# Performance work log

Hardware: AMD Instinct MI355X
Metric: run time of the kernel (lower is better)

Reference implementation:

```python
import jax, jax.numpy as jnp
import numpy as np

N_TAPS = 2
N_DELAY = 1
N_ITER = 3
EPS_MODEL = 1e-5   # LaplaceModel clamp eps (eps_models['laplace'])
EPS = 1e-3         # ISS divide/clamp eps


def mag_sq(x):
    return jnp.real(x) ** 2 + jnp.imag(x) ** 2


def laplace_weights(X):
    # Laplace source model: w[..., c, n] = 1 / (2 * ||X[..., c, :, n]||_2), broadcast over freq
    # X: (..., c, f, n) complex -> weights: (..., c, 1, n) real
    denom = 2.0 * jnp.sqrt(jnp.sum(mag_sq(X), axis=-2, keepdims=True))
    return 1.0 / jnp.maximum(denom, EPS_MODEL)


def iss_type1(src, Xc, weights):
    # Equation (9): update vector for source `src`
    Xs = Xc[..., src, :, :]  # (..., f, n)
    v_num = jnp.mean(weights * Xc * jnp.conj(Xs)[..., None, :, :], axis=-1)  # (..., c, f)
    v_denom = jnp.mean(weights * mag_sq(Xs)[..., None, :, :], axis=-1)       # (..., c, f) real
    v = v_num / jnp.maximum(v_denom, EPS)
    v_s = 1.0 - 1.0 / jnp.sqrt(jnp.maximum(v_denom[..., src, :], EPS))
    v = v.at[..., src, :].set(v_s.astype(v.dtype))
    return v


def iss_type2(src, tap, Xc, X_bar, weights):
    # update vector for dereverberation tap (src, tap)
    Xst = X_bar[..., src, :, tap, :]  # (..., f, n)
    v_num = jnp.mean(weights * Xc * jnp.conj(Xst)[..., None, :, :], axis=-1)
    # NOTE: the source code does NOT apply the 1/n_frames norm to v_denom here
    v_denom = jnp.sum(weights * mag_sq(Xst)[..., None, :, :], axis=-1)
    return v_num / jnp.maximum(v_denom, EPS)


def epoch_update(Xloc, Xc, W, X_bar, n_chan):
    weights = laplace_weights(Xloc)  # (..., c, 1, n)
    g = jnp.maximum(jnp.mean(mag_sq(Xloc), axis=(-2, -1), keepdims=True), 1e-5)
    Xloc = Xloc / jnp.sqrt(g)
    weights = weights * g
    for src in range(n_chan):
        v = iss_type1(src, Xc, weights)  # (..., c, f)
        Xc = Xc - v[..., None] * Xc[..., src, :, :][..., None, :, :]
        W = W - v[..., None] * W[..., src, :, :][..., None, :, :]
    for src in range(n_chan):
        for tap in range(N_TAPS):
            v = iss_type2(src, tap, Xc, X_bar, weights)
            Xc = Xc - v[..., None] * X_bar[..., src, :, tap, :][..., None, :, :]
    return Xloc, Xc, W


def auxiva_t_iss(X):
    batch = X.shape[:-3]
    n_chan, n_freq, n_frames = X.shape[-3:]
    T, D = N_TAPS, N_DELAY
    # hankel view of left-padded signal; keep only the T oldest rows (delayed taps)
    X_pad = jnp.pad(X, [(0, 0)] * (X.ndim - 1) + [(T + D, 0)])
    # X_bar: (..., c, f, T, n), X_bar[..., tap, t] = X[..., t - (T + D) + tap]
    X_bar = jnp.stack([X_pad[..., t:t + n_frames] for t in range(T)], axis=-2)
    eye = jnp.eye(n_chan, dtype=X.dtype)
    W = jnp.broadcast_to(eye[:, None, :], batch + (n_chan, n_freq, n_chan))
    Xloc = X  # the (buggy-but-faithful) local X that only gets renormalized each epoch
    Xc = X    # self.X, the demixed signal updated by ISS
    for _ in range(N_ITER):
        Xloc, Xc, W = epoch_update(Xloc, Xc, W, X_bar, n_chan)
    # projection back: a_f = (W_f^T)^{-1} e1 per frequency
    WT = jnp.swapaxes(jnp.swapaxes(W, -3, -2), -2, -1)  # (..., f, c, c)
    e1 = jnp.zeros((n_chan, 1), dtype=X.dtype).at[0, 0].set(1.0)
    a = jnp.linalg.solve(WT, e1)       # (..., f, c, 1)
    a = jnp.swapaxes(a, -3, -2)        # (..., c, f, 1)
    return Xc * a


def setup_inputs() -> dict:
    key = jax.random.key(0)
    k1, k2 = jax.random.split(key)
    shape = (4, 4, 257, 1024)  # (batch, n_chan, n_freq, n_frames)
    X_real = jax.random.normal(k1, shape, dtype=jnp.float32)
    X_imag = jax.random.normal(k2, shape, dtype=jnp.float32)
    return {"X_real": X_real, "X_imag": X_imag}


def reference(X_real, X_imag):
    X = jax.lax.complex(X_real, X_imag)
    return auxiva_t_iss(X)
```

## Files before the change

### kernel.cpp

```cpp
#include <hip/hip_runtime.h>
#include <math.h>

#define NB 4
#define NC 4
#define NF 257
#define NFR 1024
#define NTOT (NB * NC * NF * NFR)
#define NBC (NB * NC)
#define EPSV 1e-3f
#define EPS_MODEL 1e-5f

typedef float v2f __attribute__((ext_vector_type(2)));

__device__ float g_S[NBC * NFR];

__device__ __forceinline__ float dpp_red_sum(float v) {
  v += __int_as_float(__builtin_amdgcn_update_dpp(0, __float_as_int(v), 0x111, 0xf, 0xf, true));
  v += __int_as_float(__builtin_amdgcn_update_dpp(0, __float_as_int(v), 0x112, 0xf, 0xf, true));
  v += __int_as_float(__builtin_amdgcn_update_dpp(0, __float_as_int(v), 0x114, 0xf, 0xf, true));
  v += __int_as_float(__builtin_amdgcn_update_dpp(0, __float_as_int(v), 0x118, 0xf, 0xf, true));
  v += __int_as_float(__builtin_amdgcn_update_dpp(0, __float_as_int(v), 0x142, 0xa, 0xf, true));
  v += __int_as_float(__builtin_amdgcn_update_dpp(0, __float_as_int(v), 0x143, 0xc, 0xf, true));
  return v;
}

__global__ __launch_bounds__(256) void k_colsum(const float* __restrict__ Xr,
                                                const float* __restrict__ Xi) {
  const int bc = blockIdx.x;
  const int slice = blockIdx.y;
  const int nloc = threadIdx.x & 63;
  const int q = threadIdx.x >> 6;
  const int n = slice * 64 + nloc;

  const int f0 = q * 64;
  const int f1 = (q == 3) ? NF : (f0 + 64);

  const float* pr = Xr + (bc * NF) * NFR + n;
  const float* pi = Xi + (bc * NF) * NFR + n;
  float s = 0.f;
  for (int f = f0; f < f1; ++f) {
    float xr = pr[f * NFR];
    float xi = pi[f * NFR];
    s += xr * xr + xi * xi;
  }

  __shared__ float part[3][64];
  if (q > 0) part[q - 1][nloc] = s;
  __syncthreads();
  if (q == 0) {
    s += part[0][nloc] + part[1][nloc] + part[2][nloc];
    g_S[bc * NFR + n] = s;
  }
}

__device__ __forceinline__ void block_reduce12(float* __restrict__ p,
                                               float (*red)[2][12], int buf,
                                               int lane, int wvid,
                                               float* __restrict__ s) {
#pragma unroll
  for (int k = 0; k < 12; ++k) p[k] = dpp_red_sum(p[k]);
  if (lane == 63) {
    float4* dst = reinterpret_cast<float4*>(&red[buf][wvid][0]);
    dst[0] = make_float4(p[0], p[1], p[2], p[3]);
    dst[1] = make_float4(p[4], p[5], p[6], p[7]);
    dst[2] = make_float4(p[8], p[9], p[10], p[11]);
  }
  __syncthreads();
  const float4* r = reinterpret_cast<const float4*>(&red[buf][0][0]);
#pragma unroll
  for (int k = 0; k < 3; ++k) {
    float4 a = r[k], b = r[3 + k];
    s[4 * k + 0] = a.x + b.x;
    s[4 * k + 1] = a.y + b.y;
    s[4 * k + 2] = a.z + b.z;
    s[4 * k + 3] = a.w + b.w;
  }
}

__device__ __forceinline__ void block_reduce4(float* p, float (*red)[2][12],
                                              int buf, int lane, int wvid) {
#pragma unroll
  for (int k = 0; k < 4; ++k) p[k] = dpp_red_sum(p[k]);
  if (lane == 63) {
    float4* dst = reinterpret_cast<float4*>(&red[buf][wvid][0]);
    dst[0] = make_float4(p[0], p[1], p[2], p[3]);
  }
  __syncthreads();
  const float4* r = reinterpret_cast<const float4*>(&red[buf][0][0]);
  float4 a = r[0], b = r[3];
  p[0] = a.x + b.x;
  p[1] = a.y + b.y;
  p[2] = a.z + b.z;
  p[3] = a.w + b.w;
}

template <int SRC>
__device__ __forceinline__ void t1_sweep(v2f (&xcr)[NC][4], v2f (&xci)[NC][4],
                                         v2f (&w2)[NC][4],
                                         float (&Wre)[NC][NC], float (&Wim)[NC][NC],
                                         float (*red)[2][12], int& buf,
                                         int lane, int wvid, int tid, float invN) {
  v2f p2[12];
#pragma unroll
  for (int k = 0; k < 12; ++k) p2[k] = (v2f){0.f, 0.f};
#pragma unroll
  for (int h = 0; h < 4; ++h) {
    v2f xsr = xcr[SRC][h], xsi = xci[SRC][h];
    v2f msq = xsr * xsr + xsi * xsi;
#pragma unroll
    for (int c = 0; c < NC; ++c) {
      v2f wv = w2[c][h];
      if (c != SRC) {
        const int q = (c < SRC) ? c : c - 1;
        p2[q]     += wv * (xcr[c][h] * xsr + xci[c][h] * xsi);
        p2[3 + q] += wv * (xci[c][h] * xsr - xcr[c][h] * xsi);
      }
      p2[6 + c] += wv * msq;
    }
  }
  float p[12];
#pragma unroll
  for (int k = 0; k < 12; ++k) p[k] = p2[k].x + p2[k].y;
  float s12[12];
  block_reduce12(p, red, buf, lane, wvid, s12);
  buf ^= 1;

  float vr[NC], vi[NC];
#pragma unroll
  for (int c = 0; c < NC; ++c) {
    float den = fmaxf(s12[6 + c] * invN, EPSV);
    if (c == SRC) {
      vr[c] = 1.f - __builtin_amdgcn_rsqf(den);
      vi[c] = 0.f;
    } else {
      const int q = (c < SRC) ? c : c - 1;
      float sc = invN * __builtin_amdgcn_rcpf(den);
      vr[c] = s12[q] * sc;
      vi[c] = s12[3 + q] * sc;
    }
  }
#pragma unroll
  for (int h = 0; h < 4; ++h) {
    v2f xsr = xcr[SRC][h], xsi = xci[SRC][h];
#pragma unroll
    for (int c = 0; c < NC; ++c) {
      xcr[c][h] -= xsr * vr[c] - xsi * vi[c];
      xci[c][h] -= xsi * vr[c] + xsr * vi[c];
    }
  }
  if (tid < 16) {
    int c = tid >> 2, j = tid & 3;
    float wsr = Wre[SRC][j], wsi = Wim[SRC][j];
    float wcr = Wre[c][j],   wci = Wim[c][j];
    float vrc = (c == 0) ? vr[0] : (c == 1) ? vr[1] : (c == 2) ? vr[2] : vr[3];
    float vic = (c == 0) ? vi[0] : (c == 1) ? vi[1] : (c == 2) ? vi[2] : vi[3];
    Wre[c][j] = wcr - (vrc * wsr - vic * wsi);
    Wim[c][j] = wci - (vrc * wsi + vic * wsr);
  }
}

__global__ __launch_bounds__(128, 2) void k_main(const float* __restrict__ Xr,
                                                 const float* __restrict__ Xi,
                                                 float* __restrict__ out, int nout) {
  const int blk = blockIdx.x;
  const int b = blk / NF, f = blk % NF;
  const int tid = threadIdx.x;
  const int lane = tid & 63, wvid = tid >> 6;
  const float invN = 1.f / (float)NFR;

  __shared__ float red[2][2][12];
  __shared__ float Wre[NC][NC], Wim[NC][NC];
  __shared__ float abc[8];

  v2f xcr[NC][4], xci[NC][4];
  int rowbase[NC];
#pragma unroll
  for (int c = 0; c < NC; ++c) {
    rowbase[c] = ((b * NC + c) * NF + f) * NFR;
    const float4* pr = reinterpret_cast<const float4*>(Xr + rowbase[c]);
    const float4* pi = reinterpret_cast<const float4*>(Xi + rowbase[c]);
    float4 a0 = pr[2 * tid], a1 = pr[2 * tid + 1];
    float4 b0 = pi[2 * tid], b1 = pi[2 * tid + 1];
    xcr[c][0] = (v2f){a0.x, a0.y}; xcr[c][1] = (v2f){a0.z, a0.w};
    xcr[c][2] = (v2f){a1.x, a1.y}; xcr[c][3] = (v2f){a1.z, a1.w};
    xci[c][0] = (v2f){b0.x, b0.y}; xci[c][1] = (v2f){b0.z, b0.w};
    xci[c][2] = (v2f){b1.x, b1.y}; xci[c][3] = (v2f){b1.z, b1.w};
  }
  if (tid < 16) {
    Wre[tid >> 2][tid & 3] = ((tid >> 2) == (tid & 3)) ? 1.f : 0.f;
    Wim[tid >> 2][tid & 3] = 0.f;
  }

  int buf = 0;

  float s0v[4];
  {
    float p4[4];
#pragma unroll
    for (int c = 0; c < NC; ++c) {
      const float4* ps = reinterpret_cast<const float4*>(g_S + (b * NC + c) * NFR);
      float4 S0 = ps[2 * tid], S1 = ps[2 * tid + 1];
      p4[c] = ((S0.x + S0.y) + (S0.z + S0.w)) + ((S1.x + S1.y) + (S1.z + S1.w));
    }
    block_reduce4(p4, red, buf, lane, wvid);
    buf ^= 1;
#pragma unroll
    for (int c = 0; c < NC; ++c) s0v[c] = p4[c] / (float)(NF * NFR);
  }
  float Prun[4] = {1.f, 1.f, 1.f, 1.f};

  v2f w2[NC][4];

  for (int e = 0; e < 3; ++e) {
#pragma unroll
    for (int c = 0; c < NC; ++c) {
      float g = fmaxf(s0v[c] / Prun[c], 1e-5f);
      float sc = __builtin_amdgcn_rcpf(Prun[c]);
      Prun[c] *= g;
      const float4* ps = reinterpret_cast<const float4*>(g_S + (b * NC + c) * NFR);
      float4 S0 = ps[2 * tid], S1 = ps[2 * tid + 1];
      float sv[8] = {S0.x, S0.y, S0.z, S0.w, S1.x, S1.y, S1.z, S1.w};
      float wv[8];
#pragma unroll
      for (int j = 0; j < 8; ++j)
        wv[j] = g * __builtin_amdgcn_rcpf(fmaxf(2.f * __builtin_amdgcn_sqrtf(sv[j] * sc), EPS_MODEL));
#pragma unroll
      for (int h = 0; h < 4; ++h) w2[c][h] = (v2f){wv[2 * h], wv[2 * h + 1]};
    }

    t1_sweep<0>(xcr, xci, w2, Wre, Wim, red, buf, lane, wvid, tid, invN);
    t1_sweep<1>(xcr, xci, w2, Wre, Wim, red, buf, lane, wvid, tid, invN);
    t1_sweep<2>(xcr, xci, w2, Wre, Wim, red, buf, lane, wvid, tid, invN);
    t1_sweep<3>(xcr, xci, w2, Wre, Wim, red, buf, lane, wvid, tid, invN);

#pragma unroll 1
    for (int src = 0; src < NC; ++src) {
      const float4* pr = reinterpret_cast<const float4*>(Xr + rowbase[src]);
      const float4* pi = reinterpret_cast<const float4*>(Xi + rowbase[src]);
      float4 A4r = make_float4(0.f, 0.f, 0.f, 0.f), A4i = A4r;
      if (tid > 0) { A4r = pr[2 * tid - 1]; A4i = pi[2 * tid - 1]; }
      float4 B4r = pr[2 * tid], B4i = pi[2 * tid];
      float4 C4r = pr[2 * tid + 1], C4i = pi[2 * tid + 1];
      float wr[9] = {A4r.y, A4r.z, A4r.w, B4r.x, B4r.y, B4r.z, B4r.w, C4r.x, C4r.y};
      float wi[9] = {A4i.y, A4i.z, A4i.w, B4i.x, B4i.y, B4i.z, B4i.w, C4i.x, C4i.y};
#pragma unroll
      for (int tap = 0; tap < 2; ++tap) {
        v2f xs_r[4], xs_i[4];
#pragma unroll
        for (int h = 0; h < 4; ++h) {
          xs_r[h] = (v2f){wr[tap + 2 * h], wr[tap + 2 * h + 1]};
          xs_i[h] = (v2f){wi[tap + 2 * h], wi[tap + 2 * h + 1]};
        }
        v2f p2[12];
#pragma unroll
        for (int k = 0; k < 12; ++k) p2[k] = (v2f){0.f, 0.f};
#pragma unroll
        for (int h = 0; h < 4; ++h) {
          v2f xsr = xs_r[h], xsi = xs_i[h];
          v2f msq = xsr * xsr + xsi * xsi;
#pragma unroll
          for (int c = 0; c < NC; ++c) {
            v2f wv = w2[c][h];
            p2[c]     += wv * (xcr[c][h] * xsr + xci[c][h] * xsi);
            p2[4 + c] += wv * (xci[c][h] * xsr - xcr[c][h] * xsi);
            p2[8 + c] += wv * msq;
          }
        }
        float p[12];
#pragma unroll
        for (int k = 0; k < 12; ++k) p[k] = p2[k].x + p2[k].y;
        float s12[12];
        block_reduce12(p, red, buf, lane, wvid, s12);
        buf ^= 1;

        float vr[NC], vi[NC];
#pragma unroll
        for (int c = 0; c < NC; ++c) {
          float den = fmaxf(s12[8 + c], EPSV);
          float sc = invN * __builtin_amdgcn_rcpf(den);
          vr[c] = s12[c] * sc;
          vi[c] = s12[4 + c] * sc;
        }
#pragma unroll
        for (int h = 0; h < 4; ++h) {
          v2f xsr = xs_r[h], xsi = xs_i[h];
#pragma unroll
          for (int c = 0; c < NC; ++c) {
            xcr[c][h] -= xsr * vr[c] - xsi * vi[c];
            xci[c][h] -= xsi * vr[c] + xsr * vi[c];
          }
        }
      }
    }
  }

  __syncthreads();
  if (tid == 0) {
    float Ar[4][4], Ai[4][4];
    float br[4] = {1.f, 0.f, 0.f, 0.f}, bi[4] = {0.f, 0.f, 0.f, 0.f};
#pragma unroll
    for (int i = 0; i < 4; ++i)
#pragma unroll
      for (int j = 0; j < 4; ++j) {
        Ar[i][j] = Wre[j][i];
        Ai[i][j] = Wim[j][i];
      }
    for (int k = 0; k < 4; ++k) {
      int piv = k;
      float best = Ar[k][k] * Ar[k][k] + Ai[k][k] * Ai[k][k];
      for (int i = k + 1; i < 4; ++i) {
        float m = Ar[i][k] * Ar[i][k] + Ai[i][k] * Ai[i][k];
        if (m > best) { best = m; piv = i; }
      }
      if (piv != k) {
        for (int j = 0; j < 4; ++j) {
          float t = Ar[k][j]; Ar[k][j] = Ar[piv][j]; Ar[piv][j] = t;
          t = Ai[k][j]; Ai[k][j] = Ai[piv][j]; Ai[piv][j] = t;
        }
        float t = br[k]; br[k] = br[piv]; br[piv] = t;
        t = bi[k]; bi[k] = bi[piv]; bi[piv] = t;
      }
      float dr = Ar[k][k], di = Ai[k][k];
      float inv = 1.f / (dr * dr + di * di);
      for (int i = k + 1; i < 4; ++i) {
        float fr = (Ar[i][k] * dr + Ai[i][k] * di) * inv;
        float fi = (Ai[i][k] * dr - Ar[i][k] * di) * inv;
        for (int j = k; j < 4; ++j) {
          Ar[i][j] -= fr * Ar[k][j] - fi * Ai[k][j];
          Ai[i][j] -= fr * Ai[k][j] + fi * Ar[k][j];
        }
        br[i] -= fr * br[k] - fi * bi[k];
        bi[i] -= fr * bi[k] + fi * br[k];
      }
    }
    float ar[4], ai[4];
    for (int k = 3; k >= 0; --k) {
      float sr = br[k], si = bi[k];
      for (int j = k + 1; j < 4; ++j) {
        sr -= Ar[k][j] * ar[j] - Ai[k][j] * ai[j];
        si -= Ar[k][j] * ai[j] + Ai[k][j] * ar[j];
      }
      float dr = Ar[k][k], di = Ai[k][k];
      float inv = 1.f / (dr * dr + di * di);
      ar[k] = (sr * dr + si * di) * inv;
      ai[k] = (si * dr - sr * di) * inv;
    }
#pragma unroll
    for (int c = 0; c < 4; ++c) { abc[c] = ar[c]; abc[4 + c] = ai[c]; }
  }
  __syncthreads();

#pragma unroll
  for (int c = 0; c < NC; ++c) {
    float ar = abc[c], ai2 = abc[4 + c];
    if (rowbase[c] + 8 * tid + 7 < nout) {
      float4* po = reinterpret_cast<float4*>(out + rowbase[c]);
      v2f o0 = xcr[c][0] * ar - xci[c][0] * ai2;
      v2f o1 = xcr[c][1] * ar - xci[c][1] * ai2;
      v2f o2 = xcr[c][2] * ar - xci[c][2] * ai2;
      v2f o3 = xcr[c][3] * ar - xci[c][3] * ai2;
      po[2 * tid]     = make_float4(o0.x, o0.y, o1.x, o1.y);
      po[2 * tid + 1] = make_float4(o2.x, o2.y, o3.x, o3.y);
    }
  }
}

extern "C" void kernel_launch(void* const* d_in, const int* in_sizes, int n_in,
                              void* d_out, int out_size, void* d_ws, size_t ws_size,
                              hipStream_t stream) {
  const float* Xr = (const float*)d_in[0];
  const float* Xi = (const float*)d_in[1];
  float* out = (float*)d_out;

  dim3 g1(16, 16);
  k_colsum<<<g1, 256, 0, stream>>>(Xr, Xi);
  k_main<<<NB * NF, 128, 0, stream>>>(Xr, Xi, out, out_size);
}
```

Baseline: 201.8 us.

## Split column-sum over frequency chunks with float4 loads, cache sums in LDS

The column-sum kernel now gives each thread four frames and a 33-frequency chunk, using float4 loads, and writes 8 partial sums per column to a global scratch buffer. The main kernel adds up the partials once per block and keeps the per-frame sums in shared memory, so later epochs no longer reload them from global memory. This is meant to give the pre-pass wider, more coalesced accesses and to remove repeated global reads in the epoch loop. In exchange the main kernel reads eight times as many partials at startup and uses 16KB more LDS per block, which may lower occupancy.

```diff
diff --git a/kernel.cpp b/kernel.cpp
--- a/kernel.cpp
+++ b/kernel.cpp
@@ -9,10 +9,11 @@
 #define NBC (NB * NC)
 #define EPSV 1e-3f
 #define EPS_MODEL 1e-5f
+#define NCHUNK 8
 
 typedef float v2f __attribute__((ext_vector_type(2)));
 
-__device__ float g_S[NBC * NFR];
+__device__ float g_Spart[NCHUNK * NBC * NFR];
 
 __device__ __forceinline__ float dpp_red_sum(float v) {
   v += __int_as_float(__builtin_amdgcn_update_dpp(0, __float_as_int(v), 0x111, 0xf, 0xf, true));
@@ -27,30 +28,20 @@
 __global__ __launch_bounds__(256) void k_colsum(const float* __restrict__ Xr,
                                                 const float* __restrict__ Xi) {
   const int bc = blockIdx.x;
-  const int slice = blockIdx.y;
-  const int nloc = threadIdx.x & 63;
-  const int q = threadIdx.x >> 6;
-  const int n = slice * 64 + nloc;
-
-  const int f0 = q * 64;
-  const int f1 = (q == 3) ? NF : (f0 + 64);
-
-  const float* pr = Xr + (bc * NF) * NFR + n;
-  const float* pi = Xi + (bc * NF) * NFR + n;
-  float s = 0.f;
+  const int fc = blockIdx.y;
+  const int q = threadIdx.x;
+  int f0 = fc * 33;
+  int f1 = f0 + 33; if (f1 > NF) f1 = NF;
+  float4 s = make_float4(0.f, 0.f, 0.f, 0.f);
   for (int f = f0; f < f1; ++f) {
-    float xr = pr[f * NFR];
-    float xi = pi[f * NFR];
-    s += xr * xr + xi * xi;
-  }
-
-  __shared__ float part[3][64];
-  if (q > 0) part[q - 1][nloc] = s;
-  __syncthreads();
-  if (q == 0) {
-    s += part[0][nloc] + part[1][nloc] + part[2][nloc];
-    g_S[bc * NFR + n] = s;
-  }
+    float4 a = reinterpret_cast<const float4*>(Xr + (bc * NF + f) * NFR)[q];
+    float4 b = reinterpret_cast<const float4*>(Xi + (bc * NF + f) * NFR)[q];
+    s.x += a.x * a.x + b.x * b.x;
+    s.y += a.y * a.y + b.y * b.y;
+    s.z += a.z * a.z + b.z * b.z;
+    s.w += a.w * a.w + b.w * b.w;
+  }
+  reinterpret_cast<float4*>(g_Spart + (fc * NBC + bc) * NFR)[q] = s;
 }
 
 __device__ __forceinline__ void block_reduce12(float* __restrict__ p,
@@ -168,6 +159,7 @@
   const int lane = tid & 63, wvid = tid >> 6;
   const float invN = 1.f / (float)NFR;
 
+  __shared__ float Sown[NC][NFR];
   __shared__ float red[2][2][12];
   __shared__ float Wre[NC][NC], Wim[NC][NC];
   __shared__ float abc[8];
@@ -195,12 +187,29 @@
 
   float s0v[4];
   {
+    float acc[NC][8];
+#pragma unroll
+    for (int c = 0; c < NC; ++c)
+#pragma unroll
+      for (int j = 0; j < 8; ++j) acc[c][j] = 0.f;
+#pragma unroll 1
+    for (int fc = 0; fc < NCHUNK; ++fc) {
+#pragma unroll
+      for (int c = 0; c < NC; ++c) {
+        const float4* pp =
+            reinterpret_cast<const float4*>(g_Spart + (fc * NBC + b * NC + c) * NFR);
+        float4 a0 = pp[2 * tid], a1 = pp[2 * tid + 1];
+        acc[c][0] += a0.x; acc[c][1] += a0.y; acc[c][2] += a0.z; acc[c][3] += a0.w;
+        acc[c][4] += a1.x; acc[c][5] += a1.y; acc[c][6] += a1.z; acc[c][7] += a1.w;
+      }
+    }
     float p4[4];
 #pragma unroll
     for (int c = 0; c < NC; ++c) {
-      const float4* ps = reinterpret_cast<const float4*>(g_S + (b * NC + c) * NFR);
-      float4 S0 = ps[2 * tid], S1 = ps[2 * tid + 1];
-      p4[c] = ((S0.x + S0.y) + (S0.z + S0.w)) + ((S1.x + S1.y) + (S1.z + S1.w));
+#pragma unroll
+      for (int j = 0; j < 8; ++j) Sown[c][8 * tid + j] = acc[c][j];
+      p4[c] = ((acc[c][0] + acc[c][1]) + (acc[c][2] + acc[c][3])) +
+              ((acc[c][4] + acc[c][5]) + (acc[c][6] + acc[c][7]));
     }
     block_reduce4(p4, red, buf, lane, wvid);
     buf ^= 1;
@@ -217,13 +226,12 @@
       float g = fmaxf(s0v[c] / Prun[c], 1e-5f);
       float sc = __builtin_amdgcn_rcpf(Prun[c]);
       Prun[c] *= g;
-      const float4* ps = reinterpret_cast<const float4*>(g_S + (b * NC + c) * NFR);
-      float4 S0 = ps[2 * tid], S1 = ps[2 * tid + 1];
-      float sv[8] = {S0.x, S0.y, S0.z, S0.w, S1.x, S1.y, S1.z, S1.w};
       float wv[8];
 #pragma unroll
-      for (int j = 0; j < 8; ++j)
-        wv[j] = g * __builtin_amdgcn_rcpf(fmaxf(2.f * __builtin_amdgcn_sqrtf(sv[j] * sc), EPS_MODEL));
+      for (int j = 0; j < 8; ++j) {
+        float sv = Sown[c][8 * tid + j];
+        wv[j] = g * __builtin_amdgcn_rcpf(fmaxf(2.f * __builtin_amdgcn_sqrtf(sv * sc), EPS_MODEL));
+      }
 #pragma unroll
       for (int h = 0; h < 4; ++h) w2[c][h] = (v2f){wv[2 * h], wv[2 * h + 1]};
     }
@@ -372,7 +380,7 @@
   const float* Xi = (const float*)d_in[1];
   float* out = (float*)d_out;
 
-  dim3 g1(16, 16);
+  dim3 g1(16, NCHUNK);
   k_colsum<<<g1, 256, 0, stream>>>(Xr, Xi);
   k_main<<<NB * NF, 128, 0, stream>>>(Xr, Xi, out, out_size);
 }
```

Result: faster. 196.5 us (-2.6%).
